# Performance work log

Hardware: AMD Instinct MI355X
Metric: run time of the kernel (lower is better)

## Reference

```python
import jax, jax.numpy as jnp
import numpy as np

B, NUM, D = 8192, 8, 4096

def setup_inputs() -> dict:
    key = jax.random.key(0)
    k1, k2, k3 = jax.random.split(key, 3)
    x = jax.random.normal(k1, (B, D), dtype=jnp.float32)
    experts = jax.random.normal(k2, (B, NUM, D), dtype=jnp.float32)
    W = jax.random.normal(k3, (NUM, D), dtype=jnp.float32) * (1.0 / np.sqrt(D))
    return {"x": x, "experts": experts, "W": W}

def reference(x, experts, W):
    # gate logits: fused version of num separate Linear(input_dim,1) layers
    logits = jnp.einsum('bd,nd->bn', x, W)          # [B, num]
    weights = jax.nn.softmax(logits, axis=1)          # [B, num]
    # weighted combine of expert outputs (bmm([B,1,num],[B,num,d]).squeeze())
    return jnp.einsum('bn,bnd->bd', weights, experts) # [B, d]
```

## Files before the change

kernel.cpp:

```cpp
#include <hip/hip_runtime.h>
#include <math.h>

#define NUM_E 8
#define DIM 4096
#define THREADS 256
#define WAVES (THREADS / 64)
#define VEC_ITERS (DIM / (THREADS * 4))
#define ROWS 4

typedef float f32x4 __attribute__((ext_vector_type(4)));

__device__ __forceinline__ f32x4 nt_load4(const float* p) {
    return __builtin_nontemporal_load(reinterpret_cast<const f32x4*>(p));
}
__device__ __forceinline__ void nt_store4(float* p, f32x4 v) {
    __builtin_nontemporal_store(v, reinterpret_cast<f32x4*>(p));
}

__global__ __launch_bounds__(THREADS) void gate_fused_kernel(
    const float* __restrict__ x,
    const float* __restrict__ experts,
    const float* __restrict__ W,
    float* __restrict__ out)
{
    const int b0   = blockIdx.x * ROWS;
    const int t    = threadIdx.x;
    const int lane = t & 63;
    const int wave = t >> 6;

    __shared__ float red[ROWS][WAVES][NUM_E];

#pragma unroll
    for (int r = 0; r < ROWS; ++r) {
        const float* __restrict__ xrow = x + (size_t)(b0 + r) * DIM;
        float p[NUM_E];
#pragma unroll
        for (int n = 0; n < NUM_E; ++n) p[n] = 0.0f;

#pragma unroll
        for (int i = 0; i < VEC_ITERS; ++i) {
            const int d = (i * THREADS + t) * 4;
            const f32x4 xv = nt_load4(xrow + d);
#pragma unroll
            for (int n = 0; n < NUM_E; ++n) {
                const f32x4 wv = *reinterpret_cast<const f32x4*>(W + n * DIM + d);
                p[n] += xv.x * wv.x + xv.y * wv.y + xv.z * wv.z + xv.w * wv.w;
            }
        }

#pragma unroll
        for (int n = 0; n < NUM_E; ++n) {
#pragma unroll
            for (int off = 32; off > 0; off >>= 1)
                p[n] += __shfl_down(p[n], off, 64);
        }
        if (lane == 0) {
#pragma unroll
            for (int n = 0; n < NUM_E; ++n) red[r][wave][n] = p[n];
        }
    }
    __syncthreads();

#pragma unroll
    for (int r = 0; r < ROWS; ++r) {
        float wgt[NUM_E];
#pragma unroll
        for (int n = 0; n < NUM_E; ++n) {
            float s = 0.0f;
#pragma unroll
            for (int w2 = 0; w2 < WAVES; ++w2) s += red[r][w2][n];
            wgt[n] = s;
        }
        float m = wgt[0];
#pragma unroll
        for (int n = 1; n < NUM_E; ++n) m = fmaxf(m, wgt[n]);
        float sum = 0.0f;
#pragma unroll
        for (int n = 0; n < NUM_E; ++n) {
            wgt[n] = __expf(wgt[n] - m);
            sum += wgt[n];
        }
        const float inv = 1.0f / sum;
#pragma unroll
        for (int n = 0; n < NUM_E; ++n) wgt[n] *= inv;

        const float* __restrict__ erow = experts + (size_t)(b0 + r) * NUM_E * DIM;
        float* __restrict__ orow = out + (size_t)(b0 + r) * DIM;

#pragma unroll
        for (int i = 0; i < VEC_ITERS; ++i) {
            const int d = (i * THREADS + t) * 4;
            f32x4 acc = (f32x4)(0.0f);
#pragma unroll
            for (int n = 0; n < NUM_E; ++n) {
                const f32x4 ev = nt_load4(erow + (size_t)n * DIM + d);
                acc.x += wgt[n] * ev.x;
                acc.y += wgt[n] * ev.y;
                acc.z += wgt[n] * ev.z;
                acc.w += wgt[n] * ev.w;
            }
            nt_store4(orow + d, acc);
        }
    }
}

extern "C" void kernel_launch(void* const* d_in, const int* in_sizes, int n_in,
                              void* d_out, int out_size, void* d_ws, size_t ws_size,
                              hipStream_t stream) {
    const float* x       = (const float*)d_in[0];
    const float* experts = (const float*)d_in[1];
    const float* W       = (const float*)d_in[2];
    float* out           = (float*)d_out;

    const int B = in_sizes[0] / DIM;

    gate_fused_kernel<<<B / ROWS, THREADS, 0, stream>>>(x, experts, W, out);
}
```

Measured before the change: 248.8 us.

## Split gate softmax and expert combine into separate kernels via workspace

```diff
diff --git a/kernel.cpp b/kernel.cpp
--- a/kernel.cpp
+++ b/kernel.cpp
@@ -7,6 +7,7 @@
 #define WAVES (THREADS / 64)
 #define VEC_ITERS (DIM / (THREADS * 4))
 #define ROWS 4
+#define GRID_B 2048
 
 typedef float f32x4 __attribute__((ext_vector_type(4)));
 
@@ -17,11 +18,10 @@
     __builtin_nontemporal_store(v, reinterpret_cast<f32x4*>(p));
 }
 
-__global__ __launch_bounds__(THREADS) void gate_fused_kernel(
+__global__ __launch_bounds__(THREADS) void gate_weights_kernel(
     const float* __restrict__ x,
-    const float* __restrict__ experts,
     const float* __restrict__ W,
-    float* __restrict__ out)
+    float* __restrict__ wgt_out)
 {
     const int b0   = blockIdx.x * ROWS;
     const int t    = threadIdx.x;
@@ -47,7 +47,6 @@
                 p[n] += xv.x * wv.x + xv.y * wv.y + xv.z * wv.z + xv.w * wv.w;
             }
         }
-
 #pragma unroll
         for (int n = 0; n < NUM_E; ++n) {
 #pragma unroll
@@ -61,8 +60,8 @@
     }
     __syncthreads();
 
-#pragma unroll
-    for (int r = 0; r < ROWS; ++r) {
+    {
+        const int r = wave;
         float wgt[NUM_E];
 #pragma unroll
         for (int n = 0; n < NUM_E; ++n) {
@@ -81,11 +80,29 @@
             sum += wgt[n];
         }
         const float inv = 1.0f / sum;
-#pragma unroll
-        for (int n = 0; n < NUM_E; ++n) wgt[n] *= inv;
-
-        const float* __restrict__ erow = experts + (size_t)(b0 + r) * NUM_E * DIM;
-        float* __restrict__ orow = out + (size_t)(b0 + r) * DIM;
+        if (lane == 0) {
+#pragma unroll
+            for (int n = 0; n < NUM_E; ++n)
+                wgt_out[(size_t)(b0 + r) * NUM_E + n] = wgt[n] * inv;
+        }
+    }
+}
+
+__global__ __launch_bounds__(THREADS) void combine_kernel(
+    const float* __restrict__ experts,
+    const float* __restrict__ wgt_in,
+    float* __restrict__ out,
+    int B)
+{
+    const int t = threadIdx.x;
+
+    for (int b = blockIdx.x; b < B; b += GRID_B) {
+        const f32x4 w0 = *reinterpret_cast<const f32x4*>(wgt_in + (size_t)b * NUM_E);
+        const f32x4 w1 = *reinterpret_cast<const f32x4*>(wgt_in + (size_t)b * NUM_E + 4);
+        float wgt[NUM_E] = {w0.x, w0.y, w0.z, w0.w, w1.x, w1.y, w1.z, w1.w};
+
+        const float* __restrict__ erow = experts + (size_t)b * NUM_E * DIM;
+        float* __restrict__ orow = out + (size_t)b * DIM;
 
 #pragma unroll
         for (int i = 0; i < VEC_ITERS; ++i) {
@@ -104,6 +121,82 @@
     }
 }
 
+__global__ __launch_bounds__(THREADS) void gate_fused_kernel(
+    const float* __restrict__ x,
+    const float* __restrict__ experts,
+    const float* __restrict__ W,
+    float* __restrict__ out)
+{
+    const int b    = blockIdx.x;
+    const int t    = threadIdx.x;
+    const int lane = t & 63;
+    const int wave = t >> 6;
+
+    const float* __restrict__ xrow = x + (size_t)b * DIM;
+    const float* __restrict__ erow = experts + (size_t)b * NUM_E * DIM;
+    float* __restrict__ orow = out + (size_t)b * DIM;
+
+    float p[NUM_E];
+#pragma unroll
+    for (int n = 0; n < NUM_E; ++n) p[n] = 0.0f;
+#pragma unroll
+    for (int i = 0; i < VEC_ITERS; ++i) {
+        const int d = (i * THREADS + t) * 4;
+        const f32x4 xv = *reinterpret_cast<const f32x4*>(xrow + d);
+#pragma unroll
+        for (int n = 0; n < NUM_E; ++n) {
+            const f32x4 wv = *reinterpret_cast<const f32x4*>(W + n * DIM + d);
+            p[n] += xv.x * wv.x + xv.y * wv.y + xv.z * wv.z + xv.w * wv.w;
+        }
+    }
+#pragma unroll
+    for (int n = 0; n < NUM_E; ++n) {
+#pragma unroll
+        for (int off = 32; off > 0; off >>= 1)
+            p[n] += __shfl_down(p[n], off, 64);
+    }
+    __shared__ float red[WAVES * NUM_E];
+    if (lane == 0) {
+#pragma unroll
+        for (int n = 0; n < NUM_E; ++n) red[wave * NUM_E + n] = p[n];
+    }
+    __syncthreads();
+    float wgt[NUM_E];
+#pragma unroll
+    for (int n = 0; n < NUM_E; ++n) {
+        float s = 0.0f;
+#pragma unroll
+        for (int w2 = 0; w2 < WAVES; ++w2) s += red[w2 * NUM_E + n];
+        wgt[n] = s;
+    }
+    float m = wgt[0];
+#pragma unroll
+    for (int n = 1; n < NUM_E; ++n) m = fmaxf(m, wgt[n]);
+    float sum = 0.0f;
+#pragma unroll
+    for (int n = 0; n < NUM_E; ++n) {
+        wgt[n] = __expf(wgt[n] - m);
+        sum += wgt[n];
+    }
+    const float inv = 1.0f / sum;
+#pragma unroll
+    for (int n = 0; n < NUM_E; ++n) wgt[n] *= inv;
+#pragma unroll
+    for (int i = 0; i < VEC_ITERS; ++i) {
+        const int d = (i * THREADS + t) * 4;
+        f32x4 acc = (f32x4)(0.0f);
+#pragma unroll
+        for (int n = 0; n < NUM_E; ++n) {
+            const f32x4 ev = nt_load4(erow + (size_t)n * DIM + d);
+            acc.x += wgt[n] * ev.x;
+            acc.y += wgt[n] * ev.y;
+            acc.z += wgt[n] * ev.z;
+            acc.w += wgt[n] * ev.w;
+        }
+        nt_store4(orow + d, acc);
+    }
+}
+
 extern "C" void kernel_launch(void* const* d_in, const int* in_sizes, int n_in,
                               void* d_out, int out_size, void* d_ws, size_t ws_size,
                               hipStream_t stream) {
@@ -113,6 +206,13 @@
     float* out           = (float*)d_out;
 
     const int B = in_sizes[0] / DIM;
-
-    gate_fused_kernel<<<B / ROWS, THREADS, 0, stream>>>(x, experts, W, out);
-}
+    const size_t ws_needed = (size_t)B * NUM_E * sizeof(float);
+
+    if (ws_size >= ws_needed) {
+        float* wgt = (float*)d_ws;
+        gate_weights_kernel<<<B / ROWS, THREADS, 0, stream>>>(x, W, wgt);
+        combine_kernel<<<GRID_B, THREADS, 0, stream>>>(experts, wgt, out, B);
+    } else {
+        gate_fused_kernel<<<B, THREADS, 0, stream>>>(x, experts, W, out);
+    }
+}
```

Measured after the change: 276.3 us. 1.11x slower.

## Overlap next row's gate dot products with current row's expert combine

Applied to the files above, without the earlier changes.

```diff
diff --git a/kernel.cpp b/kernel.cpp
--- a/kernel.cpp
+++ b/kernel.cpp
@@ -4,9 +4,9 @@
 #define NUM_E 8
 #define DIM 4096
 #define THREADS 256
-#define WAVES (THREADS / 64)
+#define WAVES 4
 #define VEC_ITERS (DIM / (THREADS * 4))
-#define ROWS 4
+#define ROWS 2
 
 typedef float f32x4 __attribute__((ext_vector_type(4)));
 
@@ -17,7 +17,42 @@
     __builtin_nontemporal_store(v, reinterpret_cast<f32x4*>(p));
 }
 
-__global__ __launch_bounds__(THREADS) void gate_fused_kernel(
+__device__ __forceinline__ void reduce_softmax(float p[NUM_E],
+                                               float (*red)[NUM_E],
+                                               int lane, int wave,
+                                               float wgt[NUM_E],
+                                               bool pre_barrier)
+{
+#pragma unroll
+    for (int n = 0; n < NUM_E; ++n) {
+#pragma unroll
+        for (int off = 32; off > 0; off >>= 1)
+            p[n] += __shfl_down(p[n], off, 64);
+    }
+    if (pre_barrier) __syncthreads();
+    if (lane == 0) {
+#pragma unroll
+        for (int n = 0; n < NUM_E; ++n) red[wave][n] = p[n];
+    }
+    __syncthreads();
+#pragma unroll
+    for (int n = 0; n < NUM_E; ++n)
+        wgt[n] = red[0][n] + red[1][n] + red[2][n] + red[3][n];
+    float m = wgt[0];
+#pragma unroll
+    for (int n = 1; n < NUM_E; ++n) m = fmaxf(m, wgt[n]);
+    float sum = 0.0f;
+#pragma unroll
+    for (int n = 0; n < NUM_E; ++n) {
+        wgt[n] = __expf(wgt[n] - m);
+        sum += wgt[n];
+    }
+    const float inv = 1.0f / sum;
+#pragma unroll
+    for (int n = 0; n < NUM_E; ++n) wgt[n] *= inv;
+}
+
+__global__ __launch_bounds__(THREADS) void gate_pipelined_kernel(
     const float* __restrict__ x,
     const float* __restrict__ experts,
     const float* __restrict__ W,
@@ -28,79 +63,73 @@
     const int lane = t & 63;
     const int wave = t >> 6;
 
-    __shared__ float red[ROWS][WAVES][NUM_E];
+    __shared__ float red[WAVES][NUM_E];
+
+    const float* __restrict__ x0 = x + (size_t)b0 * DIM;
+    float p[NUM_E];
+#pragma unroll
+    for (int n = 0; n < NUM_E; ++n) p[n] = 0.0f;
+#pragma unroll
+    for (int i = 0; i < VEC_ITERS; ++i) {
+        const int d = (i * THREADS + t) * 4;
+        const f32x4 xv = nt_load4(x0 + d);
+#pragma unroll
+        for (int n = 0; n < NUM_E; ++n) {
+            const f32x4 wv = *reinterpret_cast<const f32x4*>(W + n * DIM + d);
+            p[n] += xv.x * wv.x + xv.y * wv.y + xv.z * wv.z + xv.w * wv.w;
+        }
+    }
+    float wgt0[NUM_E];
+    reduce_softmax(p, red, lane, wave, wgt0, false);
+
+    const float* __restrict__ e0 = experts + (size_t)b0 * NUM_E * DIM;
+    float* __restrict__ o0 = out + (size_t)b0 * DIM;
+    const float* __restrict__ x1 = x + (size_t)(b0 + 1) * DIM;
+
+    float p1[NUM_E];
+#pragma unroll
+    for (int n = 0; n < NUM_E; ++n) p1[n] = 0.0f;
 
 #pragma unroll
-    for (int r = 0; r < ROWS; ++r) {
-        const float* __restrict__ xrow = x + (size_t)(b0 + r) * DIM;
-        float p[NUM_E];
+    for (int i = 0; i < VEC_ITERS; ++i) {
+        const int d = (i * THREADS + t) * 4;
+        const f32x4 xv = nt_load4(x1 + d);
 #pragma unroll
-        for (int n = 0; n < NUM_E; ++n) p[n] = 0.0f;
+        for (int n = 0; n < NUM_E; ++n) {
+            const f32x4 wv = *reinterpret_cast<const f32x4*>(W + n * DIM + d);
+            p1[n] += xv.x * wv.x + xv.y * wv.y + xv.z * wv.z + xv.w * wv.w;
+        }
+        f32x4 acc = (f32x4)(0.0f);
+#pragma unroll
+        for (int n = 0; n < NUM_E; ++n) {
+            const f32x4 ev = nt_load4(e0 + (size_t)n * DIM + d);
+            acc.x += wgt0[n] * ev.x;
+            acc.y += wgt0[n] * ev.y;
+            acc.z += wgt0[n] * ev.z;
+            acc.w += wgt0[n] * ev.w;
+        }
+        nt_store4(o0 + d, acc);
+    }
+
+    float wgt1[NUM_E];
+    reduce_softmax(p1, red, lane, wave, wgt1, true);
+
+    const float* __restrict__ e1 = experts + (size_t)(b0 + 1) * NUM_E * DIM;
+    float* __restrict__ o1 = out + (size_t)(b0 + 1) * DIM;
 
 #pragma unroll
-        for (int i = 0; i < VEC_ITERS; ++i) {
-            const int d = (i * THREADS + t) * 4;
-            const f32x4 xv = nt_load4(xrow + d);
-#pragma unroll
-            for (int n = 0; n < NUM_E; ++n) {
-                const f32x4 wv = *reinterpret_cast<const f32x4*>(W + n * DIM + d);
-                p[n] += xv.x * wv.x + xv.y * wv.y + xv.z * wv.z + xv.w * wv.w;
-            }
-        }
-
+    for (int i = 0; i < VEC_ITERS; ++i) {
+        const int d = (i * THREADS + t) * 4;
+        f32x4 acc = (f32x4)(0.0f);
 #pragma unroll
         for (int n = 0; n < NUM_E; ++n) {
-#pragma unroll
-            for (int off = 32; off > 0; off >>= 1)
-                p[n] += __shfl_down(p[n], off, 64);
+            const f32x4 ev = nt_load4(e1 + (size_t)n * DIM + d);
+            acc.x += wgt1[n] * ev.x;
+            acc.y += wgt1[n] * ev.y;
+            acc.z += wgt1[n] * ev.z;
+            acc.w += wgt1[n] * ev.w;
         }
-        if (lane == 0) {
-#pragma unroll
-            for (int n = 0; n < NUM_E; ++n) red[r][wave][n] = p[n];
-        }
-    }
-    __syncthreads();
-
-#pragma unroll
-    for (int r = 0; r < ROWS; ++r) {
-        float wgt[NUM_E];
-#pragma unroll
-        for (int n = 0; n < NUM_E; ++n) {
-            float s = 0.0f;
-#pragma unroll
-            for (int w2 = 0; w2 < WAVES; ++w2) s += red[r][w2][n];
-            wgt[n] = s;
-        }
-        float m = wgt[0];
-#pragma unroll
-        for (int n = 1; n < NUM_E; ++n) m = fmaxf(m, wgt[n]);
-        float sum = 0.0f;
-#pragma unroll
-        for (int n = 0; n < NUM_E; ++n) {
-            wgt[n] = __expf(wgt[n] - m);
-            sum += wgt[n];
-        }
-        const float inv = 1.0f / sum;
-#pragma unroll
-        for (int n = 0; n < NUM_E; ++n) wgt[n] *= inv;
-
-        const float* __restrict__ erow = experts + (size_t)(b0 + r) * NUM_E * DIM;
-        float* __restrict__ orow = out + (size_t)(b0 + r) * DIM;
-
-#pragma unroll
-        for (int i = 0; i < VEC_ITERS; ++i) {
-            const int d = (i * THREADS + t) * 4;
-            f32x4 acc = (f32x4)(0.0f);
-#pragma unroll
-            for (int n = 0; n < NUM_E; ++n) {
-                const f32x4 ev = nt_load4(erow + (size_t)n * DIM + d);
-                acc.x += wgt[n] * ev.x;
-                acc.y += wgt[n] * ev.y;
-                acc.z += wgt[n] * ev.z;
-                acc.w += wgt[n] * ev.w;
-            }
-            nt_store4(orow + d, acc);
-        }
+        nt_store4(o1 + d, acc);
     }
 }
 
@@ -114,5 +143,5 @@
 
     const int B = in_sizes[0] / DIM;
 
-    gate_fused_kernel<<<B / ROWS, THREADS, 0, stream>>>(x, experts, W, out);
+    gate_pipelined_kernel<<<B / ROWS, THREADS, 0, stream>>>(x, experts, W, out);
 }
```

Result: faster. 237.5 us (-4.6%).
